# Kernel optimization log

Measured on AMD Instinct MI355X. Metric: run time of the kernel, lower is better.

Reference implementation:

```python
import jax, jax.numpy as jnp
import numpy as np
from jax import lax

CTX_SCALE = 1.0  # ctx_scale
N, RULE_DIM, E, H, V, OUT = 8192, 32, 1024, 1024, 100000, 2


def setup_inputs() -> dict:
    key = jax.random.key(0)
    ks = jax.random.split(key, 12)
    s = lambda k, shape, fan: jax.random.normal(k, shape, jnp.float32) / np.sqrt(fan)
    return {
        "rules": jax.random.normal(ks[0], (N, RULE_DIM), jnp.float32),
        "wine_id1": jax.random.randint(ks[1], (N,), 0, V),
        "wine_id2": jax.random.randint(ks[2], (N,), 0, V),
        "W_rule": s(ks[3], (RULE_DIM, E), RULE_DIM),
        "b_rule": jnp.zeros((E,), jnp.float32),
        "face_table": jax.random.normal(ks[4], (V, E), jnp.float32),
        "W_ih": s(ks[5], (4 * H, E), E),
        "W_hh": s(ks[6], (4 * H, H), H),
        "b_ih": jnp.zeros((4 * H,), jnp.float32),
        "b_hh": jnp.zeros((4 * H,), jnp.float32),
        "W_out": s(ks[7], (H, OUT), H),
        "b_out": jnp.zeros((OUT,), jnp.float32),
    }


def _lstm_cell(h, c, x, W_ih, W_hh, b_ih, b_hh):
    # torch gate order: input, forget, cell(g), output
    gates = x @ W_ih.T + b_ih + h @ W_hh.T + b_hh  # [4H]
    i, f, g, o = jnp.split(gates, 4)
    i, f, o = jax.nn.sigmoid(i), jax.nn.sigmoid(f), jax.nn.sigmoid(o)
    g = jnp.tanh(g)
    c = f * c + i * g
    h = o * jnp.tanh(c)
    return h, c


def reference(rules, wine_id1, wine_id2, W_rule, b_rule, face_table,
              W_ih, W_hh, b_ih, b_hh, W_out, b_out):
    # Embeddings for all samples at once (vectorized)
    rule_e = CTX_SCALE * (rules @ W_rule + b_rule)      # [N, E]
    f1 = face_table[wine_id1]                           # [N, E]
    f2 = face_table[wine_id2]                           # [N, E]
    xs = jnp.stack([rule_e, f1, f2], axis=1)            # [N, 3, E] ctx_order='first'

    def step(carry, x3):
        h, c = carry
        for t in range(3):  # fixed 3 timesteps per sample
            h, c = _lstm_cell(h, c, x3[t], W_ih, W_hh, b_ih, b_hh)
        out = h @ W_out + b_out                          # per-sample output
        return (h, c), out

    h0 = jnp.zeros((H,), xs.dtype)
    c0 = jnp.zeros((H,), xs.dtype)
    (h_n, c_n), outputs = lax.scan(step, (h0, c0), xs)   # outputs: [N, OUT]
    return outputs
```

## Files before the change

### kernel.cpp

```cpp
#include <hip/hip_runtime.h>

#define NS   8192
#define RD   32
#define ED   1024
#define HD   1024
#define G4   4096
#define TT   (NS * 3)
#define NBLK 128
#define RING 8

#define PAD(e) ((e) + (((e) >> 4) << 2))

__device__ __forceinline__ float sigm(float x) {
  return 1.0f / (1.0f + __expf(-x));
}
__device__ __forceinline__ float tanh_(float x) {
  float ax = fabsf(x);
  float e  = __expf(-2.0f * ax);
  float t  = (1.0f - e) / (1.0f + e);
  return x < 0.0f ? -t : t;
}

__global__ __launch_bounds__(256) void prep_kernel(
    const float* __restrict__ W_rule, const float* __restrict__ b_rule,
    const float* __restrict__ W_ih,  const float* __restrict__ b_ih,
    const float* __restrict__ b_hh,
    float* __restrict__ MT, float* __restrict__ bias0, float* __restrict__ bias12,
    unsigned long long* __restrict__ ring)
{
  int j = blockIdx.x * 256 + threadIdx.x;
  ring[(size_t)j * 2]     = 0ull;
  ring[(size_t)j * 2 + 1] = 0ull;

  float acc[RD];
  #pragma unroll
  for (int r = 0; r < RD; r++) acc[r] = 0.0f;
  float accb = 0.0f;
  const float* wrow = W_ih + (size_t)j * ED;
  for (int e = 0; e < ED; e += 4) {
    float4 w4 = *(const float4*)(wrow + e);
    float4 br = *(const float4*)(b_rule + e);
    accb += w4.x * br.x + w4.y * br.y + w4.z * br.z + w4.w * br.w;
    #pragma unroll
    for (int r = 0; r < RD; r++) {
      float4 a4 = *(const float4*)(W_rule + (size_t)r * ED + e);
      acc[r] += w4.x * a4.x + w4.y * a4.y + w4.z * a4.z + w4.w * a4.w;
    }
  }
  #pragma unroll
  for (int r = 0; r < RD; r++) MT[(size_t)j * RD + r] = acc[r];
  float bb = b_ih[j] + b_hh[j];
  bias0[j]  = accb + bb;
  bias12[j] = bb;
}

__global__ __launch_bounds__(256) void gemm_kernel(
    const float* __restrict__ A, const float* __restrict__ B,
    const float* __restrict__ bias,
    const int* __restrict__ id1, const int* __restrict__ id2,
    float* __restrict__ out, int K, int mode)
{
  __shared__ float As[32][132];
  __shared__ float Bs[32][132];
  const int t  = threadIdx.x;
  const int lr = t >> 1;
  const int lk = (t & 1) * 16;
  const int ti = t & 15;
  const int tj = t >> 4;
  const int bi = blockIdx.x, bj = blockIdx.y;

  int gi = bi * 128 + lr;
  const float* arow;
  if (mode == 0) {
    arow = A + (size_t)gi * 32;
  } else {
    int idx = (gi < NS) ? id1[gi] : id2[gi - NS];
    arow = A + (size_t)idx * ED;
  }
  const float* brow = B + (size_t)(bj * 128 + lr) * K;

  float acc[8][8];
  #pragma unroll
  for (int i = 0; i < 8; i++)
    #pragma unroll
    for (int j = 0; j < 8; j++) acc[i][j] = 0.0f;

  for (int kc = 0; kc < K; kc += 32) {
    float4 a0 = *(const float4*)(arow + kc + lk);
    float4 a1 = *(const float4*)(arow + kc + lk + 4);
    float4 a2 = *(const float4*)(arow + kc + lk + 8);
    float4 a3 = *(const float4*)(arow + kc + lk + 12);
    float4 b0 = *(const float4*)(brow + kc + lk);
    float4 b1 = *(const float4*)(brow + kc + lk + 4);
    float4 b2 = *(const float4*)(brow + kc + lk + 8);
    float4 b3 = *(const float4*)(brow + kc + lk + 12);
    __syncthreads();
    As[lk+ 0][lr]=a0.x; As[lk+ 1][lr]=a0.y; As[lk+ 2][lr]=a0.z; As[lk+ 3][lr]=a0.w;
    As[lk+ 4][lr]=a1.x; As[lk+ 5][lr]=a1.y; As[lk+ 6][lr]=a1.z; As[lk+ 7][lr]=a1.w;
    As[lk+ 8][lr]=a2.x; As[lk+ 9][lr]=a2.y; As[lk+10][lr]=a2.z; As[lk+11][lr]=a2.w;
    As[lk+12][lr]=a3.x; As[lk+13][lr]=a3.y; As[lk+14][lr]=a3.z; As[lk+15][lr]=a3.w;
    Bs[lk+ 0][lr]=b0.x; Bs[lk+ 1][lr]=b0.y; Bs[lk+ 2][lr]=b0.z; Bs[lk+ 3][lr]=b0.w;
    Bs[lk+ 4][lr]=b1.x; Bs[lk+ 5][lr]=b1.y; Bs[lk+ 6][lr]=b1.z; Bs[lk+ 7][lr]=b1.w;
    Bs[lk+ 8][lr]=b2.x; Bs[lk+ 9][lr]=b2.y; Bs[lk+10][lr]=b2.z; Bs[lk+11][lr]=b2.w;
    Bs[lk+12][lr]=b3.x; Bs[lk+13][lr]=b3.y; Bs[lk+14][lr]=b3.z; Bs[lk+15][lr]=b3.w;
    __syncthreads();
    #pragma unroll
    for (int kk = 0; kk < 32; kk++) {
      float av[8], bv[8];
      *(float4*)&av[0] = *(const float4*)&As[kk][ti * 8];
      *(float4*)&av[4] = *(const float4*)&As[kk][ti * 8 + 4];
      *(float4*)&bv[0] = *(const float4*)&Bs[kk][tj * 8];
      *(float4*)&bv[4] = *(const float4*)&Bs[kk][tj * 8 + 4];
      #pragma unroll
      for (int i = 0; i < 8; i++)
        #pragma unroll
        for (int j = 0; j < 8; j++)
          acc[i][j] += av[i] * bv[j];
    }
  }

  int j0 = bj * 128 + tj * 8;
  float bsv[8];
  *(float4*)&bsv[0] = *(const float4*)(bias + j0);
  *(float4*)&bsv[4] = *(const float4*)(bias + j0 + 4);
  int g  = j0 >> 10;
  int h0 = j0 & 1023;
  size_t pj = (size_t)(h0 >> 3) * 32 + (size_t)g * 8;
  #pragma unroll
  for (int i = 0; i < 8; i++) {
    int gi2 = bi * 128 + ti * 8 + i;
    size_t orow;
    if (mode == 0)      orow = (size_t)3 * gi2;
    else if (gi2 < NS)  orow = (size_t)3 * gi2 + 1;
    else                orow = (size_t)3 * (gi2 - NS) + 2;
    float4 o0 = make_float4(acc[i][0] + bsv[0], acc[i][1] + bsv[1],
                            acc[i][2] + bsv[2], acc[i][3] + bsv[3]);
    float4 o1 = make_float4(acc[i][4] + bsv[4], acc[i][5] + bsv[5],
                            acc[i][6] + bsv[6], acc[i][7] + bsv[7]);
    *(float4*)(out + orow * G4 + pj)     = o0;
    *(float4*)(out + orow * G4 + pj + 4) = o1;
  }
}

__global__ __launch_bounds__(512) void rnn_kernel(
    const float* __restrict__ W_hh, const float* __restrict__ xg,
    unsigned long long* ring, float* __restrict__ hhist)
{
  const int b     = blockIdx.x;
  const int tid   = threadIdx.x;
  const int wave  = tid >> 6;
  const int lane  = tid & 63;
  const int hunit = b * 8 + wave;
  const int kbase = lane * 16;

  float w[4][16];
  #pragma unroll
  for (int g = 0; g < 4; g++) {
    const float* p = W_hh + ((size_t)(g * HD + hunit)) * HD + kbase;
    *(float4*)&w[g][0]  = *(const float4*)(p);
    *(float4*)&w[g][4]  = *(const float4*)(p + 4);
    *(float4*)&w[g][8]  = *(const float4*)(p + 8);
    *(float4*)&w[g][12] = *(const float4*)(p + 12);
  }

  __shared__ float hlds[1280];
  float c = 0.0f;
  const int e0 = tid * 2;

  for (int s = 0; s < TT; s++) {
    float xgv[4] = {0.f, 0.f, 0.f, 0.f};
    if (lane == 0) {
      const float* xp = xg + (size_t)s * G4 + (size_t)b * 32;
      xgv[0] = xp[wave]; xgv[1] = xp[8 + wave];
      xgv[2] = xp[16 + wave]; xgv[3] = xp[24 + wave];
    }

    if (s == 0) {
      hlds[PAD(e0)]     = 0.0f;
      hlds[PAD(e0 + 1)] = 0.0f;
    } else {
      const unsigned long long* rrow = ring + ((size_t)((s - 1) & (RING - 1)) << 10);
      const unsigned tgt = (unsigned)s;
      unsigned long long u0, u1;
      for (;;) {
        u0 = __hip_atomic_load(&rrow[e0],     __ATOMIC_RELAXED, __HIP_MEMORY_SCOPE_AGENT);
        u1 = __hip_atomic_load(&rrow[e0 + 1], __ATOMIC_RELAXED, __HIP_MEMORY_SCOPE_AGENT);
        if ((unsigned)(u0 >> 32) == tgt && (unsigned)(u1 >> 32) == tgt) break;
        __builtin_amdgcn_s_sleep(1);
      }
      hlds[PAD(e0)]     = __uint_as_float((unsigned)u0);
      hlds[PAD(e0 + 1)] = __uint_as_float((unsigned)u1);
    }
    __syncthreads();

    float hq[16];
    const float* hp = &hlds[lane * 20];
    *(float4*)&hq[0]  = *(const float4*)(hp);
    *(float4*)&hq[4]  = *(const float4*)(hp + 4);
    *(float4*)&hq[8]  = *(const float4*)(hp + 8);
    *(float4*)&hq[12] = *(const float4*)(hp + 12);

    float si = 0.f, sf = 0.f, sg = 0.f, so = 0.f;
    #pragma unroll
    for (int q = 0; q < 16; q++) {
      float h = hq[q];
      si += w[0][q] * h; sf += w[1][q] * h;
      sg += w[2][q] * h; so += w[3][q] * h;
    }
    #pragma unroll
    for (int off = 32; off > 0; off >>= 1) {
      si += __shfl_down(si, off);
      sf += __shfl_down(sf, off);
      sg += __shfl_down(sg, off);
      so += __shfl_down(so, off);
    }

    if (lane == 0) {
      float iv = sigm(si + xgv[0]);
      float fv = sigm(sf + xgv[1]);
      float gv = tanh_(sg + xgv[2]);
      float ov = sigm(so + xgv[3]);
      c = fv * c + iv * gv;
      float hv = ov * tanh_(c);
      unsigned long long pk =
          ((unsigned long long)(unsigned)(s + 1) << 32) |
          (unsigned long long)__float_as_uint(hv);
      __hip_atomic_store(&ring[((size_t)(s & (RING - 1)) << 10) + hunit], pk,
                         __ATOMIC_RELAXED, __HIP_MEMORY_SCOPE_AGENT);
      if (s % 3 == 2) hhist[(size_t)(s / 3) * HD + hunit] = hv;
    }
    __syncthreads();
  }
}

__global__ __launch_bounds__(256) void out_kernel(
    const float* __restrict__ hhist, const float* __restrict__ W_out,
    const float* __restrict__ b_out, float* __restrict__ out)
{
  int n = blockIdx.x;
  int tid = threadIdx.x;
  const float* h = hhist + (size_t)n * HD;
  int k0 = tid * 4;
  float4 h4 = *(const float4*)(h + k0);
  float4 wa = *(const float4*)(W_out + (size_t)k0 * 2);
  float4 wb = *(const float4*)(W_out + (size_t)k0 * 2 + 4);
  float a0 = h4.x * wa.x + h4.y * wa.z + h4.z * wb.x + h4.w * wb.z;
  float a1 = h4.x * wa.y + h4.y * wa.w + h4.z * wb.y + h4.w * wb.w;
  #pragma unroll
  for (int off = 32; off > 0; off >>= 1) {
    a0 += __shfl_down(a0, off);
    a1 += __shfl_down(a1, off);
  }
  __shared__ float r0[4], r1[4];
  if ((tid & 63) == 0) { r0[tid >> 6] = a0; r1[tid >> 6] = a1; }
  __syncthreads();
  if (tid == 0) {
    out[(size_t)n * 2 + 0] = r0[0] + r0[1] + r0[2] + r0[3] + b_out[0];
    out[(size_t)n * 2 + 1] = r1[0] + r1[1] + r1[2] + r1[3] + b_out[1];
  }
}

extern "C" void kernel_launch(void* const* d_in, const int* in_sizes, int n_in,
                              void* d_out, int out_size, void* d_ws, size_t ws_size,
                              hipStream_t stream) {
  const float* rules  = (const float*)d_in[0];
  const int*   id1    = (const int*)  d_in[1];
  const int*   id2    = (const int*)  d_in[2];
  const float* W_rule = (const float*)d_in[3];
  const float* b_rule = (const float*)d_in[4];
  const float* face   = (const float*)d_in[5];
  const float* W_ih   = (const float*)d_in[6];
  const float* W_hh   = (const float*)d_in[7];
  const float* b_ih   = (const float*)d_in[8];
  const float* b_hh   = (const float*)d_in[9];
  const float* W_out  = (const float*)d_in[10];
  const float* b_out  = (const float*)d_in[11];
  float* out = (float*)d_out;

  float* xg     = (float*)d_ws;
  float* MT     = xg + (size_t)TT * G4;
  float* bias0  = MT + (size_t)G4 * RD;
  float* bias12 = bias0 + G4;
  float* hhist  = bias12 + G4;
  unsigned long long* ring = (unsigned long long*)(hhist + (size_t)NS * HD);

  prep_kernel<<<dim3(G4 / 256), dim3(256), 0, stream>>>(
      W_rule, b_rule, W_ih, b_ih, b_hh, MT, bias0, bias12, ring);

  gemm_kernel<<<dim3(NS / 128, G4 / 128), dim3(256), 0, stream>>>(
      rules, MT, bias0, id1, id2, xg, 32, 0);

  gemm_kernel<<<dim3(2 * NS / 128, G4 / 128), dim3(256), 0, stream>>>(
      face, W_ih, bias12, id1, id2, xg, ED, 1);

  rnn_kernel<<<dim3(NBLK), dim3(512), 0, stream>>>(W_hh, xg, ring, hhist);

  out_kernel<<<dim3(NS), dim3(256), 0, stream>>>(hhist, W_out, b_out, out);
}
```

Before: 70.39 ms.

## Double-buffer LDS h, drop trailing barrier, DPP reductions, pipelined ring polling

Moves the hidden-state staging buffer to two alternating LDS halves so the second __syncthreads per timestep can be removed. Replaces the shuffle-based wave reductions with DPP row-shift and row-broadcast adds, which leave the result in lane 63, so the gate computation moves to that lane. The spin-wait on the cross-block ring now keeps three loads in flight to shorten polling latency. This targets per-step latency in the serial recurrence, but the stale-load pipelining and the single barrier per step change the ordering assumptions the loop relies on.

```diff
diff --git a/kernel.cpp b/kernel.cpp
--- a/kernel.cpp
+++ b/kernel.cpp
@@ -11,6 +11,8 @@
 
 #define PAD(e) ((e) + (((e) >> 4) << 2))
 
+#define RLOAD(p) __hip_atomic_load((p), __ATOMIC_RELAXED, __HIP_MEMORY_SCOPE_AGENT)
+
 __device__ __forceinline__ float sigm(float x) {
   return 1.0f / (1.0f + __expf(-x));
 }
@@ -19,6 +21,21 @@
   float e  = __expf(-2.0f * ax);
   float t  = (1.0f - e) / (1.0f + e);
   return x < 0.0f ? -t : t;
+}
+
+template <int CTRL, int RMASK>
+__device__ __forceinline__ float dpp_add(float x) {
+  int v = __builtin_amdgcn_update_dpp(0, __float_as_int(x), CTRL, RMASK, 0xf, true);
+  return x + __int_as_float(v);
+}
+__device__ __forceinline__ float wave_reduce63(float x) {
+  x = dpp_add<0x111, 0xf>(x);
+  x = dpp_add<0x112, 0xf>(x);
+  x = dpp_add<0x114, 0xf>(x);
+  x = dpp_add<0x118, 0xf>(x);
+  x = dpp_add<0x142, 0xa>(x);
+  x = dpp_add<0x143, 0xc>(x);
+  return x;
 }
 
 __global__ __launch_bounds__(256) void prep_kernel(
@@ -163,38 +180,40 @@
     *(float4*)&w[g][12] = *(const float4*)(p + 12);
   }
 
-  __shared__ float hlds[1280];
+  __shared__ float hlds[2][1280];
   float c = 0.0f;
   const int e0 = tid * 2;
 
   for (int s = 0; s < TT; s++) {
+    const int cur = s & 1;
+
     float xgv[4] = {0.f, 0.f, 0.f, 0.f};
-    if (lane == 0) {
+    if (lane == 63) {
       const float* xp = xg + (size_t)s * G4 + (size_t)b * 32;
       xgv[0] = xp[wave]; xgv[1] = xp[8 + wave];
       xgv[2] = xp[16 + wave]; xgv[3] = xp[24 + wave];
     }
 
     if (s == 0) {
-      hlds[PAD(e0)]     = 0.0f;
-      hlds[PAD(e0 + 1)] = 0.0f;
+      *(float2*)&hlds[cur][PAD(e0)] = make_float2(0.0f, 0.0f);
     } else {
       const unsigned long long* rrow = ring + ((size_t)((s - 1) & (RING - 1)) << 10);
       const unsigned tgt = (unsigned)s;
-      unsigned long long u0, u1;
-      for (;;) {
-        u0 = __hip_atomic_load(&rrow[e0],     __ATOMIC_RELAXED, __HIP_MEMORY_SCOPE_AGENT);
-        u1 = __hip_atomic_load(&rrow[e0 + 1], __ATOMIC_RELAXED, __HIP_MEMORY_SCOPE_AGENT);
-        if ((unsigned)(u0 >> 32) == tgt && (unsigned)(u1 >> 32) == tgt) break;
+      unsigned long long a0 = RLOAD(&rrow[e0]), a1 = RLOAD(&rrow[e0 + 1]);
+      unsigned long long b0 = RLOAD(&rrow[e0]), b1 = RLOAD(&rrow[e0 + 1]);
+      unsigned long long c0 = RLOAD(&rrow[e0]), c1 = RLOAD(&rrow[e0 + 1]);
+      while (!((unsigned)(a0 >> 32) == tgt && (unsigned)(a1 >> 32) == tgt)) {
+        a0 = b0; a1 = b1; b0 = c0; b1 = c1;
+        c0 = RLOAD(&rrow[e0]); c1 = RLOAD(&rrow[e0 + 1]);
         __builtin_amdgcn_s_sleep(1);
       }
-      hlds[PAD(e0)]     = __uint_as_float((unsigned)u0);
-      hlds[PAD(e0 + 1)] = __uint_as_float((unsigned)u1);
+      *(float2*)&hlds[cur][PAD(e0)] =
+          make_float2(__uint_as_float((unsigned)a0), __uint_as_float((unsigned)a1));
     }
     __syncthreads();
 
     float hq[16];
-    const float* hp = &hlds[lane * 20];
+    const float* hp = &hlds[cur][lane * 20];
     *(float4*)&hq[0]  = *(const float4*)(hp);
     *(float4*)&hq[4]  = *(const float4*)(hp + 4);
     *(float4*)&hq[8]  = *(const float4*)(hp + 8);
@@ -207,15 +226,12 @@
       si += w[0][q] * h; sf += w[1][q] * h;
       sg += w[2][q] * h; so += w[3][q] * h;
     }
-    #pragma unroll
-    for (int off = 32; off > 0; off >>= 1) {
-      si += __shfl_down(si, off);
-      sf += __shfl_down(sf, off);
-      sg += __shfl_down(sg, off);
-      so += __shfl_down(so, off);
-    }
-
-    if (lane == 0) {
+    si = wave_reduce63(si);
+    sf = wave_reduce63(sf);
+    sg = wave_reduce63(sg);
+    so = wave_reduce63(so);
+
+    if (lane == 63) {
       float iv = sigm(si + xgv[0]);
       float fv = sigm(sf + xgv[1]);
       float gv = tanh_(sg + xgv[2]);
@@ -229,7 +245,6 @@
                          __ATOMIC_RELAXED, __HIP_MEMORY_SCOPE_AGENT);
       if (s % 3 == 2) hhist[(size_t)(s / 3) * HD + hunit] = hv;
     }
-    __syncthreads();
   }
 }
 
```

Result: slower. 89.17 ms (+26.7%).
